# Performance work log

Measured on AMD Instinct MI355X. Metric: run time of the kernel, lower is better.

Reference implementation:

```python
import jax, jax.numpy as jnp
import numpy as np
import math

B, D_IN, D_MODEL, N_LAYERS, N_HALF, D_OUT = 32, 100, 256, 4, 32, 1
K_ENC = 64               # ConvTranspose2d kernel -> 64x64 feature map from 1x1 latent
L_SEQ = K_ENC * K_ENC    # 4096 flattened spatial sequence for S4D
DT_MIN, DT_MAX = 0.001, 0.1


def setup_inputs() -> dict:
    key = jax.random.key(0)
    ks = jax.random.split(key, 8)
    x = jax.random.normal(ks[0], (B, D_IN, 1, 1), jnp.float32)
    # encoder ConvTranspose2d weight: (in, out, kh, kw)
    enc_w = jax.random.normal(ks[1], (D_IN, D_MODEL, K_ENC, K_ENC), jnp.float32) * 0.02
    # S4D kernel params per layer (stacked over layers)
    log_dt = math.log(DT_MIN) + jax.random.uniform(ks[2], (N_LAYERS, D_MODEL), jnp.float32) * (
        math.log(DT_MAX) - math.log(DT_MIN))
    C = jax.random.normal(ks[3], (N_LAYERS, D_MODEL, N_HALF, 2), jnp.float32)  # complex C as (re, im)
    log_A_real = jnp.log(0.5 * jnp.ones((N_LAYERS, D_MODEL, N_HALF), jnp.float32))
    A_imag = jnp.tile(math.pi * jnp.arange(N_HALF, dtype=jnp.float32), (N_LAYERS, D_MODEL, 1))
    Dskip = jax.random.normal(ks[4], (N_LAYERS, D_MODEL), jnp.float32)
    # output_linear: Conv1d(H, 2H, 1) followed by GLU(dim=-2)
    out_w = jax.random.normal(ks[5], (N_LAYERS, 2 * D_MODEL, D_MODEL), jnp.float32) / math.sqrt(D_MODEL)
    out_b = jnp.zeros((N_LAYERS, 2 * D_MODEL), jnp.float32)
    # decoder: Conv2d(d_model, d_output, 1)
    dec_w = jax.random.normal(ks[6], (D_OUT, D_MODEL), jnp.float32) / math.sqrt(D_MODEL)
    dec_b = jnp.zeros((D_OUT,), jnp.float32)
    return dict(x=x, enc_w=enc_w, log_dt=log_dt, C=C, log_A_real=log_A_real,
                A_imag=A_imag, Dskip=Dskip, out_w=out_w, out_b=out_b,
                dec_w=dec_w, dec_b=dec_b)


def s4d_kernel(log_dt, C, log_A_real, A_imag, L):
    """S4D convolution kernel via Vandermonde: returns (H, L) real kernel."""
    dt = jnp.exp(log_dt)                       # (H,)
    Cc = C[..., 0] + 1j * C[..., 1]            # (H, N)
    A = -jnp.exp(log_A_real) + 1j * A_imag     # (H, N) diagonal state matrix
    dtA = A * dt[:, None]                      # (H, N)
    V = jnp.exp(dtA[:, :, None] * jnp.arange(L, dtype=log_dt.dtype))  # (H, N, L) Vandermonde
    Cc = Cc * (jnp.exp(dtA) - 1.0) / A         # ZOH discretization of C
    return 2.0 * jnp.einsum('hn,hnl->hl', Cc, V).real  # (H, L)


def s4d_layer(u, log_dt, C, log_A_real, A_imag, Dskip, out_w, out_b):
    """u: (B, H, L) -> (B, H, L). FFT convolution + skip + GELU + 1x1 conv + GLU."""
    L = u.shape[-1]
    k = s4d_kernel(log_dt, C, log_A_real, A_imag, L)
    k_f = jnp.fft.rfft(k, n=2 * L)             # (H, L+1)
    u_f = jnp.fft.rfft(u, n=2 * L)             # (B, H, L+1)
    y = jnp.fft.irfft(u_f * k_f, n=2 * L)[..., :L]
    y = y + u * Dskip[:, None]
    y = jax.nn.gelu(y, approximate=False)      # torch nn.GELU (exact erf)
    y = jnp.einsum('oh,bhl->bol', out_w, y) + out_b[:, None]  # Conv1d(H, 2H, 1)
    a, b = jnp.split(y, 2, axis=1)             # GLU along channel dim
    return a * jax.nn.sigmoid(b)


def reference(x, enc_w, log_dt, C, log_A_real, A_imag, Dskip, out_w, out_b, dec_w, dec_b):
    # encoder: ConvTranspose2d(kernel=64, stride=4, bias=False) on a 1x1 input
    # is exactly an outer product of latent with the kernel.
    h = jnp.einsum('bixy,iohw->bohw', x, enc_w)        # (B, D_MODEL, 64, 64)
    Bb, Hc, Hh, Ww = h.shape
    h = h.reshape(Bb, Hc, Hh * Ww)                     # (B, H, L) flattened spatial sequence
    for i in range(N_LAYERS):                          # prenorm=False -> no LayerNorm applied
        z = s4d_layer(h, log_dt[i], C[i], log_A_real[i], A_imag[i],
                      Dskip[i], out_w[i], out_b[i])
        h = z + h                                      # residual
    y = jnp.einsum('oc,bcl->bol', dec_w, h) + dec_b[:, None]  # Conv2d 1x1 decoder
    return y.reshape(Bb, D_OUT, Hh, Ww)
```

## Files before the change

kernel.cpp:

```cpp
#include <hip/hip_runtime.h>
#include <hip/hip_bf16.h>
#include <math.h>

#define BB   32
#define DIN  100
#define HH   256
#define NLAY 4
#define NH   32
#define LL   4096
#define LC   128
#define NC   32
#define HL   (HH*LL)
#define BLn  (BB*LL)

typedef __attribute__((ext_vector_type(8))) short s8v;
typedef __attribute__((ext_vector_type(4))) float f4v;

__device__ inline unsigned short f2b(float x) {
    unsigned int u = __float_as_uint(x);
    unsigned int r = (u + 0x7fffu + ((u >> 16) & 1u)) >> 16;
    return (unsigned short)r;
}
__device__ inline float b2f(unsigned short u) {
    return __uint_as_float(((unsigned int)u) << 16);
}

__global__ __launch_bounds__(256) void k_enc(const float* __restrict__ x,
                                             const float* __restrict__ ew,
                                             unsigned short* __restrict__ hb) {
    __shared__ unsigned short xs[BB*128];
    __shared__ unsigned short ot[BB*264];
    int tid = threadIdx.x;
    for (int idx = tid; idx < BB*128; idx += 256) {
        int b = idx >> 7, k = idx & 127;
        float v = (k < DIN) ? x[b*DIN + k] : 0.f;
        int slot = (k >> 3) ^ (b & 7);
        xs[b*128 + slot*8 + (k & 7)] = f2b(v);
    }
    __syncthreads();
    int hl0 = blockIdx.x * 256;
    int h = hl0 >> 12, l0 = hl0 & 4095;
    int w = tid >> 6, l = tid & 63;
    int l16 = l & 15, lk8 = (l >> 4) * 8, e4 = (l >> 4) * 4;
    int col0 = w * 64;
    f4v acc[2][4];
    #pragma unroll
    for (int i = 0; i < 2; i++)
        #pragma unroll
        for (int j = 0; j < 4; j++) acc[i][j] = (f4v){0.f,0.f,0.f,0.f};
    #pragma unroll
    for (int ks = 0; ks < 4; ks++) {
        int kb = ks*32 + lk8;
        int sl0 = kb >> 3;
        s8v a0 = *(const s8v*)&xs[l16*128 + (sl0 ^ (l16 & 7))*8];
        s8v a1 = *(const s8v*)&xs[(16 + l16)*128 + (sl0 ^ (l16 & 7))*8];
        #pragma unroll
        for (int j = 0; j < 4; j++) {
            int hl = hl0 + col0 + j*16 + l16;
            const float* ep = ew + (size_t)kb * HL + hl;
            s8v bf;
            #pragma unroll
            for (int q = 0; q < 8; q++) {
                float ev = (kb + q < DIN) ? ep[(size_t)q * HL] : 0.f;
                bf[q] = (short)f2b(ev);
            }
            acc[0][j] = __builtin_amdgcn_mfma_f32_16x16x32_bf16(a0, bf, acc[0][j], 0, 0, 0);
            acc[1][j] = __builtin_amdgcn_mfma_f32_16x16x32_bf16(a1, bf, acc[1][j], 0, 0, 0);
        }
    }
    #pragma unroll
    for (int i = 0; i < 2; i++)
        #pragma unroll
        for (int j = 0; j < 4; j++) {
            int cl = col0 + j*16 + l16;
            #pragma unroll
            for (int e = 0; e < 4; e++) {
                int b = i*16 + e4 + e;
                ot[b*264 + cl] = f2b(acc[i][j][e]);
            }
        }
    __syncthreads();
    {
        int b = tid >> 3, off = (tid & 7) * 32;
        const unsigned short* src = &ot[b*264 + off];
        unsigned short* dst = &hb[(size_t)h*BLn + (size_t)b*LL + l0 + off];
        #pragma unroll
        for (int q = 0; q < 4; q++)
            *(s8v*)(dst + q*8) = *(const s8v*)(src + q*8);
    }
}

__global__ __launch_bounds__(256) void k_prep1(const float* __restrict__ ldt,
        const float* __restrict__ Cp, const float* __restrict__ lAr,
        const float* __restrict__ Aimp,
        float* __restrict__ pdta, float* __restrict__ pwlc, float* __restrict__ pcd2) {
    int g = blockIdx.x*256 + threadIdx.x;
    int layer = g >> 13, h = (g >> 5) & 255, n = g & 31;
    float dt  = expf(ldt[layer*HH + h]);
    float are = -expf(lAr[(layer*HH + h)*NH + n]);
    float aim = Aimp[(layer*HH + h)*NH + n];
    float dre = are*dt, dimg = aim*dt;
    float er = expf(dre);
    float s, c; sincosf(dimg, &s, &c);
    float wre = er*c, wim = er*s;
    float den = are*are + aim*aim;
    float nre = wre - 1.f, nim = wim;
    float qre = (nre*are + nim*aim)/den;
    float qim = (nim*are - nre*aim)/den;
    float cre = Cp[((layer*HH + h)*NH + n)*2 + 0];
    float cim = Cp[((layer*HH + h)*NH + n)*2 + 1];
    float dcr = cre*qre - cim*qim;
    float dci = cre*qim + cim*qre;
    pcd2[g*2+0] = 2.f*dcr;  pcd2[g*2+1] = 2.f*dci;
    pdta[g*2+0] = dre;      pdta[g*2+1] = dimg;
    float erl = expf(dre*(float)LC);
    float sl, cl; sincosf(dimg*(float)LC, &sl, &cl);
    pwlc[g*2+0] = erl*cl;   pwlc[g*2+1] = erl*sl;
}

__global__ __launch_bounds__(256) void k_bldAll(const float* __restrict__ pdta,
        const float* __restrict__ pcd2, unsigned short* __restrict__ AstB,
        unsigned short* __restrict__ AcvB) {
    __shared__ float dre_s[NH], dim_s[NH], c2r[NH], c2i[NH];
    __shared__ float kkl[LC];
    int bid = blockIdx.x;
    int tid = threadIdx.x;
    int pbase = bid * 64;
    if (tid < NH) {
        dre_s[tid] = pdta[pbase + tid*2];
        dim_s[tid] = pdta[pbase + tid*2 + 1];
        c2r[tid]   = pcd2[pbase + tid*2];
        c2i[tid]   = pcd2[pbase + tid*2 + 1];
    }
    __syncthreads();
    if (tid < LC) {
        float fm = (float)tid;
        float acc = 0.f;
        for (int n = 0; n < NH; n++) {
            float er = expf(dre_s[n]*fm);
            float s, c; sincosf(dim_s[n]*fm, &s, &c);
            acc += c2r[n]*er*c - c2i[n]*er*s;
        }
        kkl[tid] = acc;
    }
    __syncthreads();
    unsigned short* As = AstB + (size_t)bid * 8192;
    for (int idx = tid; idx < 8192; idx += 256) {
        int r = idx >> 7, m = idx & 127, n = r >> 1;
        float e = (float)(127 - m);
        float er = expf(dre_s[n]*e);
        float s, c; sincosf(dim_s[n]*e, &s, &c);
        As[idx] = f2b((r & 1) ? er*s : er*c);
    }
    unsigned short* Ac = AcvB + (size_t)bid * 24576;
    for (int idx = tid; idx < 24576; idx += 256) {
        int j = idx / 192, k = idx - j*192;
        float v;
        if (k < 128) {
            v = (j >= k) ? kkl[j - k] : 0.f;
        } else {
            int n = (k - 128) >> 1;
            float e = (float)(j + 1);
            float er = expf(dre_s[n]*e);
            float s, c; sincosf(dim_s[n]*e, &s, &c);
            v = ((k - 128) & 1) ? (-er*s) : (er*c);
        }
        Ac[idx] = f2b(v);
    }
}

__global__ __launch_bounds__(256) void k_prepW(const float* __restrict__ outw,
                                               unsigned short* __restrict__ Wbf) {
    int t = blockIdx.x*256 + threadIdx.x;
    Wbf[t] = f2b(outw[t]);
}

__global__ __launch_bounds__(256) void k_BG(const unsigned short* __restrict__ AstB,
        const unsigned short* __restrict__ AcvB, const unsigned short* __restrict__ hb,
        const float* __restrict__ pwlc, const float* __restrict__ pcd2,
        const float* __restrict__ DskL, unsigned short* __restrict__ Ybf) {
    __shared__ unsigned short Ul[128*128];
    __shared__ unsigned short Fl[128*64];
    int ct = blockIdx.x, h = blockIdx.y;
    int tid = threadIdx.x;
    const unsigned short* ub = hb + (size_t)h*BLn + (size_t)ct*128*LC;
    #pragma unroll
    for (int it = 0; it < 8; it++) {
        int idx = it*256 + tid;
        int col = idx >> 4, slot = idx & 15;
        s8v v = *(const s8v*)(ub + col*LC + slot*8);
        *(s8v*)&Ul[col*128 + (slot ^ (col & 7))*8] = v;
    }
    __syncthreads();
    int w = tid >> 6, l = tid & 63;
    int l16 = l & 15, lk8 = (l >> 4)*8, e4 = (l >> 4)*4;
    int k8q = l >> 4;

    {
        f4v acc[8];
        #pragma unroll
        for (int j = 0; j < 8; j++) acc[j] = (f4v){0.f,0.f,0.f,0.f};
        const unsigned short* Ab = AstB + (size_t)h*8192 + (w*16 + l16)*128;
        #pragma unroll
        for (int ks = 0; ks < 4; ks++) {
            s8v af = *(const s8v*)(Ab + ks*32 + lk8);
            int k8 = ks*4 + k8q;
            #pragma unroll
            for (int j = 0; j < 8; j++) {
                int col = j*16 + l16;
                s8v bf = *(const s8v*)&Ul[col*128 + (k8 ^ (col & 7))*8];
                acc[j] = __builtin_amdgcn_mfma_f32_16x16x32_bf16(af, bf, acc[j], 0, 0, 0);
            }
        }
        #pragma unroll
        for (int j = 0; j < 8; j++) {
            int col = j*16 + l16;
            int idx = (col*64 + w*16 + e4) ^ ((col & 7) << 3);
            *(ushort4*)&Fl[idx] = make_ushort4(f2b(acc[j][0]), f2b(acc[j][1]),
                                               f2b(acc[j][2]), f2b(acc[j][3]));
        }
    }
    __syncthreads();

    if (tid < 128) {
        int n = tid & 31, bl = tid >> 5;
        int hn2 = (h*NH + n)*2;
        float wlr = pwlc[hn2], wli = pwlc[hn2+1];
        float cr  = pcd2[hn2], ci  = pcd2[hn2+1];
        float sr = 0.f, si = 0.f;
        #pragma unroll 4
        for (int c = 0; c < NC; c++) {
            int lcol = bl*32 + c;
            int idx = (lcol*64 + 2*n) ^ ((lcol & 7) << 3);
            ushort2 fv = *(ushort2*)&Fl[idx];
            float fr = b2f(fv.x), fi = b2f(fv.y);
            *(ushort2*)&Fl[idx] = make_ushort2(f2b(cr*sr - ci*si), f2b(cr*si + ci*sr));
            float nsr = fmaf(wlr, sr, fmaf(-wli, si, fr));
            si = fmaf(wlr, si, fmaf(wli, sr, fi));
            sr = nsr;
        }
    }
    __syncthreads();

    float dsk = DskL[h];
    const unsigned short* Cb = AcvB + (size_t)h*24576;
    f4v acc[2][8];
    #pragma unroll
    for (int i = 0; i < 2; i++)
        #pragma unroll
        for (int j = 0; j < 8; j++) acc[i][j] = (f4v){0.f,0.f,0.f,0.f};
    #pragma unroll
    for (int ks = 0; ks < 4; ks++) {
        s8v af0 = *(const s8v*)(Cb + (w*32 + l16)*192 + ks*32 + lk8);
        s8v af1 = *(const s8v*)(Cb + (w*32 + 16 + l16)*192 + ks*32 + lk8);
        int k8 = ks*4 + k8q;
        #pragma unroll
        for (int j = 0; j < 8; j++) {
            int col = j*16 + l16;
            s8v bf = *(const s8v*)&Ul[col*128 + (k8 ^ (col & 7))*8];
            acc[0][j] = __builtin_amdgcn_mfma_f32_16x16x32_bf16(af0, bf, acc[0][j], 0, 0, 0);
            acc[1][j] = __builtin_amdgcn_mfma_f32_16x16x32_bf16(af1, bf, acc[1][j], 0, 0, 0);
        }
    }
    #pragma unroll
    for (int ks = 0; ks < 2; ks++) {
        s8v af0 = *(const s8v*)(Cb + (w*32 + l16)*192 + 128 + ks*32 + lk8);
        s8v af1 = *(const s8v*)(Cb + (w*32 + 16 + l16)*192 + 128 + ks*32 + lk8);
        int kk2 = ks*32 + lk8;
        #pragma unroll
        for (int j = 0; j < 8; j++) {
            int col = j*16 + l16;
            int idx = (col*64 + kk2) ^ ((col & 7) << 3);
            s8v bf = *(const s8v*)&Fl[idx];
            acc[0][j] = __builtin_amdgcn_mfma_f32_16x16x32_bf16(af0, bf, acc[0][j], 0, 0, 0);
            acc[1][j] = __builtin_amdgcn_mfma_f32_16x16x32_bf16(af1, bf, acc[1][j], 0, 0, 0);
        }
    }
    unsigned short* Yb = Ybf + (size_t)h*BLn + (size_t)ct*128*LC;
    #pragma unroll
    for (int i = 0; i < 2; i++) {
        int m0 = w*32 + i*16 + e4;
        int sl = m0 >> 3, off = m0 & 7;
        #pragma unroll
        for (int j = 0; j < 8; j++) {
            int col = j*16 + l16;
            ushort4 u4 = *(const ushort4*)&Ul[col*128 + (sl ^ (col & 7))*8 + off];
            float uu[4] = {b2f(u4.x), b2f(u4.y), b2f(u4.z), b2f(u4.w)};
            unsigned short ov[4];
            #pragma unroll
            for (int e = 0; e < 4; e++) {
                float yv = acc[i][j][e] + dsk*uu[e];
                ov[e] = f2b(0.5f*yv*(1.f + erff(yv*0.70710678118f)));
            }
            *(ushort4*)&Yb[col*LC + m0] = make_ushort4(ov[0], ov[1], ov[2], ov[3]);
        }
    }
}

__global__ __launch_bounds__(512) void k_gC2(const unsigned short* __restrict__ Wb,
        const float* __restrict__ outb, const unsigned short* __restrict__ Ybf,
        unsigned short* __restrict__ hb, const float* __restrict__ dw,
        const float* __restrict__ db, float* __restrict__ outp, int doDec) {
    __shared__ __align__(16) unsigned char smem[34048];
    unsigned short* Bl = (unsigned short*)smem;
    float* part = (float*)smem;
    int nt = blockIdx.x;
    int n0 = nt*64;
    int tid = threadIdx.x;

    {
        int jn = (tid & 15) * 4;
        int hq = tid >> 4;
        #pragma unroll
        for (int hb8 = 0; hb8 < 8; hb8++) {
            int h = hb8*32 + hq;
            ushort4 v = *(const ushort4*)&Ybf[(size_t)h*BLn + n0 + jn];
            unsigned short vv[4] = {v.x, v.y, v.z, v.w};
            #pragma unroll
            for (int i = 0; i < 4; i++) {
                int row = jn + i;
                Bl[row*258 + (h ^ ((row & 7) << 3))] = vv[i];
            }
        }
    }
    __syncthreads();

    int w = tid >> 6, l = tid & 63;
    int l16 = l & 15, lk8 = (l >> 4) * 8, e4 = (l >> 4) * 4;
    int ra = w*32 + l16;
    int swz = (l16 & 7) << 3;
    f4v acc[4][4];
    #pragma unroll
    for (int i = 0; i < 4; i++)
        #pragma unroll
        for (int j = 0; j < 4; j++) acc[i][j] = (f4v){0.f,0.f,0.f,0.f};
    const unsigned short* W0 = Wb + ra*HH;
    const unsigned short* W1 = Wb + (ra+16)*HH;
    const unsigned short* W2 = Wb + (ra+256)*HH;
    const unsigned short* W3 = Wb + (ra+272)*HH;
    #pragma unroll
    for (int ks = 0; ks < 8; ks++) {
        int kk = ks*32 + lk8;
        s8v a0 = *(const s8v*)(W0 + kk);
        s8v a1 = *(const s8v*)(W1 + kk);
        s8v a2 = *(const s8v*)(W2 + kk);
        s8v a3 = *(const s8v*)(W3 + kk);
        s8v bfv[4];
        #pragma unroll
        for (int j = 0; j < 4; j++) {
            int row = j*16 + l16;
            bfv[j] = *(const s8v*)&Bl[row*258 + (kk ^ swz)];
        }
        #pragma unroll
        for (int j = 0; j < 4; j++) {
            acc[0][j] = __builtin_amdgcn_mfma_f32_16x16x32_bf16(a0, bfv[j], acc[0][j], 0, 0, 0);
            acc[1][j] = __builtin_amdgcn_mfma_f32_16x16x32_bf16(a1, bfv[j], acc[1][j], 0, 0, 0);
            acc[2][j] = __builtin_amdgcn_mfma_f32_16x16x32_bf16(a2, bfv[j], acc[2][j], 0, 0, 0);
            acc[3][j] = __builtin_amdgcn_mfma_f32_16x16x32_bf16(a3, bfv[j], acc[3][j], 0, 0, 0);
        }
    }

    float pj[4] = {0.f, 0.f, 0.f, 0.f};
    #pragma unroll
    for (int i = 0; i < 2; i++) {
        int ob = w*32 + i*16 + e4;
        #pragma unroll
        for (int e = 0; e < 4; e++) {
            int o = ob + e;
            float ba  = outb[o];
            float bb2 = outb[o + 256];
            float dwo = doDec ? dw[o] : 0.f;
            #pragma unroll
            for (int j = 0; j < 4; j++) {
                float za = acc[i][j][e] + ba;
                float zb = acc[i+2][j][e] + bb2;
                float sig = 1.f/(1.f + expf(-zb));
                unsigned short* hp = &hb[(size_t)o*BLn + n0 + j*16 + l16];
                float hnew = b2f(*hp) + za*sig;
                if (doDec) {
                    pj[j] = fmaf(dwo, hnew, pj[j]);
                } else {
                    *hp = f2b(hnew);
                }
            }
        }
    }

    if (doDec) {
        __syncthreads();
        int g32 = w*4 + (l >> 4);
        #pragma unroll
        for (int j = 0; j < 4; j++) {
            int nl = j*16 + l16;
            part[nl*33 + g32] = pj[j];
        }
        __syncthreads();
        if (tid < 64) {
            float s = db[0];
            #pragma unroll
            for (int g = 0; g < 32; g++) s += part[tid*33 + g];
            outp[n0 + tid] = s;
        }
    }
}

extern "C" void kernel_launch(void* const* d_in, const int* in_sizes, int n_in,
                              void* d_out, int out_size, void* d_ws, size_t ws_size,
                              hipStream_t stream) {
    (void)in_sizes; (void)n_in; (void)out_size; (void)ws_size;
    const float* x    = (const float*)d_in[0];
    const float* ew   = (const float*)d_in[1];
    const float* ldt  = (const float*)d_in[2];
    const float* Cp   = (const float*)d_in[3];
    const float* lAr  = (const float*)d_in[4];
    const float* Aimp = (const float*)d_in[5];
    const float* Dsk  = (const float*)d_in[6];
    const float* outw = (const float*)d_in[7];
    const float* outb = (const float*)d_in[8];
    const float* dw   = (const float*)d_in[9];
    const float* db   = (const float*)d_in[10];

    float* ws = (float*)d_ws;
    unsigned short* hb  = (unsigned short*)ws;
    unsigned short* Ybf = (unsigned short*)(ws + 16777216UL);
    unsigned short* AstB= (unsigned short*)(ws + 33554432UL);
    unsigned short* AcvB= (unsigned short*)(ws + 37748736UL);
    unsigned short* Wbf = (unsigned short*)(ws + 50331648UL);
    float* pdta = ws + 50593792UL;
    float* pwlc = ws + 50659328UL;
    float* pcd2 = ws + 50724864UL;

    k_prep1<<<128, 256, 0, stream>>>(ldt, Cp, lAr, Aimp, pdta, pwlc, pcd2);
    k_bldAll<<<1024, 256, 0, stream>>>(pdta, pcd2, AstB, AcvB);
    k_prepW<<<2048, 256, 0, stream>>>(outw, Wbf);
    k_enc<<<4096, 256, 0, stream>>>(x, ew, hb);
    for (int layer = 0; layer < NLAY; layer++) {
        k_BG<<<dim3(8, 256), 256, 0, stream>>>(AstB + (size_t)layer*2097152,
                                               AcvB + (size_t)layer*6291456, hb,
                                               pwlc + layer*16384, pcd2 + layer*16384,
                                               Dsk + layer*HH, Ybf);
        k_gC2<<<2048, 512, 0, stream>>>(Wbf + layer*131072, outb + layer*512, Ybf, hb,
                                        dw, db, (float*)d_out, (layer == NLAY-1) ? 1 : 0);
    }
}
```

Before: 993.0 us.

## Stage S4D and GLU outputs through LDS for coalesced global writes

k_BG now transposes its GELU output through shared memory so each thread writes 16-byte contiguous rows instead of scattered 8-byte stores. Its 2D grid is flattened with a block-index remap that interleaves heads across XCDs. k_gC2 stages the GLU result through LDS in two passes so the residual read-modify-write of hb uses vectorised contiguous accesses instead of 2-byte scattered ones, and the decoder flag becomes a template parameter. Together these target uncoalesced global memory traffic, at the cost of extra barriers and LDS round trips.

```diff
diff --git a/kernel.cpp b/kernel.cpp
--- a/kernel.cpp
+++ b/kernel.cpp
@@ -179,9 +179,13 @@
         const unsigned short* __restrict__ AcvB, const unsigned short* __restrict__ hb,
         const float* __restrict__ pwlc, const float* __restrict__ pcd2,
         const float* __restrict__ DskL, unsigned short* __restrict__ Ybf) {
-    __shared__ unsigned short Ul[128*128];
-    __shared__ unsigned short Fl[128*64];
-    int ct = blockIdx.x, h = blockIdx.y;
+    __shared__ __align__(16) unsigned short smem[24576];
+    unsigned short* Ul = smem;
+    unsigned short* Fl = smem + 16384;
+    unsigned short* zt = smem;
+    int g = blockIdx.x;
+    int h  = (g & 7)*32 + ((g >> 3) & 31);
+    int ct = g >> 8;
     int tid = threadIdx.x;
     const unsigned short* ub = hb + (size_t)h*BLn + (size_t)ct*128*LC;
     #pragma unroll
@@ -193,13 +197,12 @@
     }
     __syncthreads();
     int w = tid >> 6, l = tid & 63;
-    int l16 = l & 15, lk8 = (l >> 4)*8, e4 = (l >> 4)*4;
-    int k8q = l >> 4;
+    int l16 = l & 15, lk8 = (l >> 4)*8, e4 = (l >> 4)*4, k8q = l >> 4;
 
     {
-        f4v acc[8];
-        #pragma unroll
-        for (int j = 0; j < 8; j++) acc[j] = (f4v){0.f,0.f,0.f,0.f};
+        f4v facc[8];
+        #pragma unroll
+        for (int j = 0; j < 8; j++) facc[j] = (f4v){0.f,0.f,0.f,0.f};
         const unsigned short* Ab = AstB + (size_t)h*8192 + (w*16 + l16)*128;
         #pragma unroll
         for (int ks = 0; ks < 4; ks++) {
@@ -209,15 +212,15 @@
             for (int j = 0; j < 8; j++) {
                 int col = j*16 + l16;
                 s8v bf = *(const s8v*)&Ul[col*128 + (k8 ^ (col & 7))*8];
-                acc[j] = __builtin_amdgcn_mfma_f32_16x16x32_bf16(af, bf, acc[j], 0, 0, 0);
+                facc[j] = __builtin_amdgcn_mfma_f32_16x16x32_bf16(af, bf, facc[j], 0, 0, 0);
             }
         }
         #pragma unroll
         for (int j = 0; j < 8; j++) {
             int col = j*16 + l16;
             int idx = (col*64 + w*16 + e4) ^ ((col & 7) << 3);
-            *(ushort4*)&Fl[idx] = make_ushort4(f2b(acc[j][0]), f2b(acc[j][1]),
-                                               f2b(acc[j][2]), f2b(acc[j][3]));
+            *(ushort4*)&Fl[idx] = make_ushort4(f2b(facc[j][0]), f2b(facc[j][1]),
+                                               f2b(facc[j][2]), f2b(facc[j][3]));
         }
     }
     __syncthreads();
@@ -276,7 +279,7 @@
             acc[1][j] = __builtin_amdgcn_mfma_f32_16x16x32_bf16(af1, bf, acc[1][j], 0, 0, 0);
         }
     }
-    unsigned short* Yb = Ybf + (size_t)h*BLn + (size_t)ct*128*LC;
+    ushort4 ovr[16];
     #pragma unroll
     for (int i = 0; i < 2; i++) {
         int m0 = w*32 + i*16 + e4;
@@ -292,17 +295,42 @@
                 float yv = acc[i][j][e] + dsk*uu[e];
                 ov[e] = f2b(0.5f*yv*(1.f + erff(yv*0.70710678118f)));
             }
-            *(ushort4*)&Yb[col*LC + m0] = make_ushort4(ov[0], ov[1], ov[2], ov[3]);
-        }
-    }
-}
-
+            ovr[i*8+j] = make_ushort4(ov[0], ov[1], ov[2], ov[3]);
+        }
+    }
+    __syncthreads();
+    #pragma unroll
+    for (int i = 0; i < 2; i++) {
+        int m0 = w*32 + i*16 + e4;
+        #pragma unroll
+        for (int j = 0; j < 8; j++) {
+            int col = j*16 + l16;
+            *(ushort4*)&zt[col*132 + m0] = ovr[i*8+j];
+        }
+    }
+    __syncthreads();
+    {
+        int colR = tid >> 1, mseg = (tid & 1) * 64;
+        unsigned short* Yb = Ybf + (size_t)h*BLn + (size_t)(ct*128 + colR)*LC;
+        #pragma unroll
+        for (int q = 0; q < 8; q++) {
+            ushort4 a = *(const ushort4*)&zt[colR*132 + mseg + q*8];
+            ushort4 b = *(const ushort4*)&zt[colR*132 + mseg + q*8 + 4];
+            union { s8v v; ushort4 u[2]; } pk;
+            pk.u[0] = a; pk.u[1] = b;
+            *(s8v*)(Yb + mseg + q*8) = pk.v;
+        }
+    }
+}
+
+template<int DEC>
 __global__ __launch_bounds__(512) void k_gC2(const unsigned short* __restrict__ Wb,
         const float* __restrict__ outb, const unsigned short* __restrict__ Ybf,
         unsigned short* __restrict__ hb, const float* __restrict__ dw,
-        const float* __restrict__ db, float* __restrict__ outp, int doDec) {
-    __shared__ __align__(16) unsigned char smem[34048];
+        const float* __restrict__ db, float* __restrict__ outp) {
+    __shared__ __align__(16) unsigned char smem[33792];
     unsigned short* Bl = (unsigned short*)smem;
+    float* zt   = (float*)smem;
     float* part = (float*)smem;
     int nt = blockIdx.x;
     int n0 = nt*64;
@@ -360,45 +388,67 @@
         }
     }
 
-    float pj[4] = {0.f, 0.f, 0.f, 0.f};
-    #pragma unroll
-    for (int i = 0; i < 2; i++) {
-        int ob = w*32 + i*16 + e4;
-        #pragma unroll
-        for (int e = 0; e < 4; e++) {
-            int o = ob + e;
-            float ba  = outb[o];
-            float bb2 = outb[o + 256];
-            float dwo = doDec ? dw[o] : 0.f;
-            #pragma unroll
-            for (int j = 0; j < 4; j++) {
-                float za = acc[i][j][e] + ba;
-                float zb = acc[i+2][j][e] + bb2;
-                float sig = 1.f/(1.f + expf(-zb));
-                unsigned short* hp = &hb[(size_t)o*BLn + n0 + j*16 + l16];
-                float hnew = b2f(*hp) + za*sig;
-                if (doDec) {
-                    pj[j] = fmaf(dwo, hnew, pj[j]);
+    int rrow = tid >> 2;
+    int cseg = (tid & 3) * 16;
+    float pj[16];
+    if (DEC) {
+        #pragma unroll
+        for (int c = 0; c < 16; c++) pj[c] = 0.f;
+    }
+    #pragma unroll
+    for (int pass = 0; pass < 2; pass++) {
+        __syncthreads();
+        if ((w >> 2) == pass) {
+            #pragma unroll
+            for (int i = 0; i < 2; i++) {
+                #pragma unroll
+                for (int e = 0; e < 4; e++) {
+                    int o  = w*32 + i*16 + e4 + e;
+                    int ol = o - pass*128;
+                    float ba  = outb[o];
+                    float bb2 = outb[o + 256];
+                    #pragma unroll
+                    for (int j = 0; j < 4; j++) {
+                        float za = acc[i][j][e] + ba;
+                        float zb = acc[i+2][j][e] + bb2;
+                        float sig = 1.f/(1.f + expf(-zb));
+                        zt[ol*66 + j*16 + l16] = za*sig;
+                    }
+                }
+            }
+        }
+        __syncthreads();
+        {
+            int hrow = pass*128 + rrow;
+            float dwv = DEC ? dw[hrow] : 0.f;
+            unsigned short* hp = &hb[(size_t)hrow*BLn + n0 + cseg];
+            #pragma unroll
+            for (int q = 0; q < 4; q++) {
+                ushort4 hv = *(ushort4*)(hp + q*4);
+                float f0 = b2f(hv.x) + zt[rrow*66 + cseg + q*4 + 0];
+                float f1 = b2f(hv.y) + zt[rrow*66 + cseg + q*4 + 1];
+                float f2 = b2f(hv.z) + zt[rrow*66 + cseg + q*4 + 2];
+                float f3 = b2f(hv.w) + zt[rrow*66 + cseg + q*4 + 3];
+                if (DEC) {
+                    pj[q*4+0] = fmaf(dwv, f0, pj[q*4+0]);
+                    pj[q*4+1] = fmaf(dwv, f1, pj[q*4+1]);
+                    pj[q*4+2] = fmaf(dwv, f2, pj[q*4+2]);
+                    pj[q*4+3] = fmaf(dwv, f3, pj[q*4+3]);
                 } else {
-                    *hp = f2b(hnew);
+                    *(ushort4*)(hp + q*4) = make_ushort4(f2b(f0), f2b(f1), f2b(f2), f2b(f3));
                 }
             }
         }
     }
-
-    if (doDec) {
+    if (DEC) {
         __syncthreads();
-        int g32 = w*4 + (l >> 4);
-        #pragma unroll
-        for (int j = 0; j < 4; j++) {
-            int nl = j*16 + l16;
-            part[nl*33 + g32] = pj[j];
-        }
+        #pragma unroll
+        for (int c = 0; c < 16; c++)
+            part[rrow*66 + cseg + c] = pj[c];
         __syncthreads();
         if (tid < 64) {
             float s = db[0];
-            #pragma unroll
-            for (int g = 0; g < 32; g++) s += part[tid*33 + g];
+            for (int g2 = 0; g2 < 128; g2++) s += part[g2*66 + tid];
             outp[n0 + tid] = s;
         }
     }
@@ -435,11 +485,15 @@
     k_prepW<<<2048, 256, 0, stream>>>(outw, Wbf);
     k_enc<<<4096, 256, 0, stream>>>(x, ew, hb);
     for (int layer = 0; layer < NLAY; layer++) {
-        k_BG<<<dim3(8, 256), 256, 0, stream>>>(AstB + (size_t)layer*2097152,
-                                               AcvB + (size_t)layer*6291456, hb,
-                                               pwlc + layer*16384, pcd2 + layer*16384,
-                                               Dsk + layer*HH, Ybf);
-        k_gC2<<<2048, 512, 0, stream>>>(Wbf + layer*131072, outb + layer*512, Ybf, hb,
-                                        dw, db, (float*)d_out, (layer == NLAY-1) ? 1 : 0);
-    }
-}
+        k_BG<<<2048, 256, 0, stream>>>(AstB + (size_t)layer*2097152,
+                                       AcvB + (size_t)layer*6291456, hb,
+                                       pwlc + layer*16384, pcd2 + layer*16384,
+                                       Dsk + layer*HH, Ybf);
+        if (layer < NLAY-1)
+            k_gC2<0><<<2048, 512, 0, stream>>>(Wbf + layer*131072, outb + layer*512,
+                                               Ybf, hb, dw, db, (float*)d_out);
+        else
+            k_gC2<1><<<2048, 512, 0, stream>>>(Wbf + layer*131072, outb + layer*512,
+                                               Ybf, hb, dw, db, (float*)d_out);
+    }
+}
```

Result: slower. 1.055 ms (+6.3%).
